# Performance work log

Hardware: AMD Instinct MI355X
Metric: run time of the kernel (lower is better)

Reference implementation:

```python
import jax, jax.numpy as jnp
import numpy as np

# dims: T tokens, HID hidden, H heads, D head_dim, K conv kernel size
T, HID, H, D, K = 4096, 2048, 16, 128, 4
HD = H * D
EPS = 1e-6


def causal_conv(x, w):
    # depthwise causal conv: x [T, C], w [C, K]; y_t = sum_i w[:, i] * x_{t-K+1+i}
    xp = jnp.pad(x, ((K - 1, 0), (0, 0)))
    y = jnp.zeros_like(x)
    for i in range(K):  # small fixed kernel loop
        y = y + w[:, i] * xp[i:i + x.shape[0]]
    return y


def l2norm(x):
    return x * jax.lax.rsqrt(jnp.sum(x * x, -1, keepdims=True) + EPS)


def setup_inputs() -> dict:
    key = jax.random.key(0)
    ks = jax.random.split(key, 16)
    s = lambda n: 1.0 / np.sqrt(n)
    return {
        "hidden_states": jax.random.normal(ks[0], (T, HID), jnp.float32),
        "Wq": jax.random.normal(ks[1], (HID, HD), jnp.float32) * s(HID),
        "Wk": jax.random.normal(ks[2], (HID, HD), jnp.float32) * s(HID),
        "Wv": jax.random.normal(ks[3], (HID, HD), jnp.float32) * s(HID),
        "wq_conv": jax.random.normal(ks[4], (HD, K), jnp.float32) * s(K),
        "wk_conv": jax.random.normal(ks[5], (HD, K), jnp.float32) * s(K),
        "wv_conv": jax.random.normal(ks[6], (HD, K), jnp.float32) * s(K),
        "A_log": jax.random.uniform(ks[7], (H,), jnp.float32, 0.0, 0.5),
        "dt_bias": jax.random.normal(ks[8], (HD,), jnp.float32) * 0.1,
        "Wfa": jax.random.normal(ks[9], (HID, D), jnp.float32) * s(HID),
        "Wfb": jax.random.normal(ks[10], (D, HD), jnp.float32) * s(D),
        "Wb": jax.random.normal(ks[11], (HID, H), jnp.float32) * s(HID),
        "Wga": jax.random.normal(ks[12], (HID, D), jnp.float32) * s(HID),
        "Wgb": jax.random.normal(ks[13], (D, HD), jnp.float32) * s(D),
        "norm_w": jnp.ones((D,), jnp.float32),
        "Wo": jax.random.normal(ks[14], (HD, HID), jnp.float32) * s(HD),
    }


def reference(hidden_states, Wq, Wk, Wv, wq_conv, wk_conv, wv_conv, A_log,
              dt_bias, Wfa, Wfb, Wb, Wga, Wgb, norm_w, Wo):
    x = hidden_states
    # projections + short causal conv + SiLU
    q = jax.nn.silu(causal_conv(x @ Wq, wq_conv)).reshape(T, H, D)
    k = jax.nn.silu(causal_conv(x @ Wk, wk_conv)).reshape(T, H, D)
    v = jax.nn.silu(causal_conv(x @ Wv, wv_conv)).reshape(T, H, D)
    # fine-grained per-channel log-decay: g = -exp(A_log) * softplus(f + dt_bias), [T,H,D]
    f = (x @ Wfa) @ Wfb + dt_bias
    g = -(jnp.exp(A_log)[None, :, None]) * jax.nn.softplus(f.reshape(T, H, D))
    beta = jax.nn.sigmoid(x @ Wb)  # [T, H]
    q = l2norm(q)
    k = l2norm(k)
    scale = D ** -0.5

    def step(S, inp):  # S: [H, Dk, Dv]
        q_t, k_t, v_t, g_t, b_t = inp
        S = S * jnp.exp(g_t)[..., None]  # diagonal per-key-channel decay
        err = v_t - jnp.einsum('hkv,hk->hv', S, k_t)  # delta-rule error
        dv = b_t[:, None] * err  # beta gate
        S = S + k_t[:, :, None] * dv[:, None, :]
        o_t = jnp.einsum('hkv,hk->hv', S, q_t) * scale
        return S, o_t

    S0 = jnp.zeros((H, D, D), jnp.float32)
    _, o = jax.lax.scan(step, S0, (q, k, v, g, beta))  # o: [T, H, D]

    # gated RMSNorm then output projection
    gate = ((x @ Wga) @ Wgb).reshape(T, H, D)
    o = o * jax.lax.rsqrt(jnp.mean(o * o, -1, keepdims=True) + EPS)
    o = o * norm_w * jax.nn.silu(gate)
    return o.reshape(T, HD) @ Wo
```

## Files before the change

kernel.cpp:

```cpp
#include <hip/hip_runtime.h>
#include <hip/hip_bf16.h>
#include <math.h>

typedef __bf16 bf16_t;
typedef __bf16 bf16x8 __attribute__((ext_vector_type(8)));
typedef float  floatx4 __attribute__((ext_vector_type(4)));
typedef float  floatx2 __attribute__((ext_vector_type(2)));
typedef unsigned uintx4 __attribute__((ext_vector_type(4)));

constexpr int T_TOK = 4096;
constexpr int HID   = 2048;
constexpr int NH    = 16;
constexpr int DH    = 128;
constexpr int CH    = 2048;
constexpr int CHUNK = 16;
constexpr int NCH   = T_TOK / CHUNK;

__global__ __launch_bounds__(256) void cast_to_bf16(const float* __restrict__ in,
                                                    bf16_t* __restrict__ out, int n) {
  int i = (blockIdx.x * 256 + threadIdx.x) * 8;
  if (i >= n) return;
  float4 a = *(const float4*)(in + i);
  float4 b = *(const float4*)(in + i + 4);
  bf16x8 o;
  o[0]=(bf16_t)a.x; o[1]=(bf16_t)a.y; o[2]=(bf16_t)a.z; o[3]=(bf16_t)a.w;
  o[4]=(bf16_t)b.x; o[5]=(bf16_t)b.y; o[6]=(bf16_t)b.z; o[7]=(bf16_t)b.w;
  *(bf16x8*)(out + i) = o;
}

__global__ __launch_bounds__(256) void transpose_cast(const float* __restrict__ in,
                                                      bf16_t* __restrict__ out, int R, int C) {
  __shared__ float tile[32][33];
  int tx = threadIdx.x & 31;
  int ty = threadIdx.x >> 5;
  int r0 = blockIdx.x * 32;
  int c0 = blockIdx.y * 32;
#pragma unroll
  for (int i = 0; i < 4; i++) {
    int r = ty + i * 8;
    float v = 0.f;
    if (r0 + r < R && c0 + tx < C) v = in[(size_t)(r0 + r) * C + (c0 + tx)];
    tile[r][tx] = v;
  }
  __syncthreads();
#pragma unroll
  for (int i = 0; i < 4; i++) {
    int cr = ty + i * 8;
    if (c0 + cr < C && r0 + tx < R)
      out[(size_t)(c0 + cr) * R + (r0 + tx)] = (bf16_t)tile[tx][cr];
  }
}

template<bool OUT_BF16>
__global__ __launch_bounds__(256) void gemm_bf16(
    const bf16_t* __restrict__ A, int lda,
    const bf16_t* __restrict__ Bt, int ldb,
    void* __restrict__ Cv, int ldc, int M, int N, int K) {
  __shared__ bf16_t sA[128][40];
  __shared__ bf16_t sB[128][40];
  const int tid  = threadIdx.x;
  const int bm0  = blockIdx.x * 128;
  const int bn0  = blockIdx.y * 128;
  const int wave = tid >> 6;
  const int lane = tid & 63;
  const int wm   = (wave & 1) * 64;
  const int wn   = (wave >> 1) * 64;
  const int fm   = lane & 15;
  const int kq   = lane >> 4;

  floatx4 acc[4][4];
#pragma unroll
  for (int mi = 0; mi < 4; mi++)
#pragma unroll
    for (int ni = 0; ni < 4; ni++)
      acc[mi][ni] = (floatx4){0.f, 0.f, 0.f, 0.f};

  const int sr = tid >> 2;
  const int sk = (tid & 3) * 8;
  const bool bval0 = (bn0 + sr) < N;
  const bool bval1 = (bn0 + sr + 64) < N;
  const bf16_t* Ag0 = A + (size_t)(bm0 + sr) * lda + sk;
  const bf16_t* Ag1 = Ag0 + (size_t)64 * lda;
  const bf16_t* Bg0 = Bt + (size_t)(bn0 + sr) * ldb + sk;
  const bf16_t* Bg1 = Bg0 + (size_t)64 * ldb;

  for (int k0 = 0; k0 < K; k0 += 32) {
    float4 a0 = *(const float4*)(Ag0 + k0);
    float4 a1 = *(const float4*)(Ag1 + k0);
    float4 b0 = bval0 ? *(const float4*)(Bg0 + k0) : make_float4(0.f, 0.f, 0.f, 0.f);
    float4 b1 = bval1 ? *(const float4*)(Bg1 + k0) : make_float4(0.f, 0.f, 0.f, 0.f);
    __syncthreads();
    *(float4*)(&sA[sr][sk])      = a0;
    *(float4*)(&sA[sr + 64][sk]) = a1;
    *(float4*)(&sB[sr][sk])      = b0;
    *(float4*)(&sB[sr + 64][sk]) = b1;
    __syncthreads();
    bf16x8 afr[4], bfr[4];
#pragma unroll
    for (int i = 0; i < 4; i++) {
      afr[i] = *(const bf16x8*)(&sA[wm + i * 16 + fm][kq * 8]);
      bfr[i] = *(const bf16x8*)(&sB[wn + i * 16 + fm][kq * 8]);
    }
#pragma unroll
    for (int mi = 0; mi < 4; mi++)
#pragma unroll
      for (int ni = 0; ni < 4; ni++)
        acc[mi][ni] = __builtin_amdgcn_mfma_f32_16x16x32_bf16(afr[mi], bfr[ni], acc[mi][ni], 0, 0, 0);
  }

  const int rr = (lane >> 4) * 4;
#pragma unroll
  for (int mi = 0; mi < 4; mi++) {
#pragma unroll
    for (int r = 0; r < 4; r++) {
      const int row = bm0 + wm + mi * 16 + rr + r;
#pragma unroll
      for (int ni = 0; ni < 4; ni++) {
        const int col = bn0 + wn + ni * 16 + fm;
        if (col < N) {
          if constexpr (OUT_BF16)
            ((bf16_t*)Cv)[(size_t)row * ldc + col] = (bf16_t)acc[mi][ni][r];
          else
            ((float*)Cv)[(size_t)row * ldc + col] = acc[mi][ni][r];
        }
      }
    }
  }
}

__device__ __forceinline__ void gload_lds16(const bf16_t* g, bf16_t* l) {
  __builtin_amdgcn_global_load_lds(
      (const __attribute__((address_space(1))) void*)g,
      (__attribute__((address_space(3))) void*)l, 16, 0, 0);
}

template<bool OUT_BF16>
__global__ __launch_bounds__(256) void gemm_bf16_lds(
    const bf16_t* __restrict__ A, int lda,
    const bf16_t* __restrict__ Bt, int ldb,
    void* __restrict__ Cv, int ldc, int M, int N, int K) {
  __shared__ bf16_t sA[128][32];
  __shared__ bf16_t sB[128][32];
  const int tid  = threadIdx.x;
  const int bm0  = blockIdx.x * 128;
  const int bn0  = blockIdx.y * 128;
  const int wave = tid >> 6;
  const int lane = tid & 63;
  const int wm   = (wave & 1) * 64;
  const int wn   = (wave >> 1) * 64;
  const int fm   = lane & 15;
  const int kq   = lane >> 4;

  floatx4 acc[4][4];
#pragma unroll
  for (int mi = 0; mi < 4; mi++)
#pragma unroll
    for (int ni = 0; ni < 4; ni++)
      acc[mi][ni] = (floatx4){0.f, 0.f, 0.f, 0.f};

  const int sr = tid >> 2;
  const int sk = (tid & 3) * 8;
  const bf16_t* Ag0 = A + (size_t)(bm0 + sr) * lda + sk;
  const bf16_t* Ag1 = Ag0 + (size_t)64 * lda;
  const bf16_t* Bg0 = Bt + (size_t)(bn0 + sr) * ldb + sk;
  const bf16_t* Bg1 = Bg0 + (size_t)64 * ldb;
  bf16_t* ldsA0 = &sA[16 * wave][0];
  bf16_t* ldsA1 = &sA[64 + 16 * wave][0];
  bf16_t* ldsB0 = &sB[16 * wave][0];
  bf16_t* ldsB1 = &sB[64 + 16 * wave][0];

  for (int k0 = 0; k0 < K; k0 += 32) {
    __syncthreads();
    gload_lds16(Ag0 + k0, ldsA0);
    gload_lds16(Ag1 + k0, ldsA1);
    gload_lds16(Bg0 + k0, ldsB0);
    gload_lds16(Bg1 + k0, ldsB1);
    __syncthreads();
    bf16x8 afr[4], bfr[4];
#pragma unroll
    for (int i = 0; i < 4; i++) {
      afr[i] = *(const bf16x8*)(&sA[wm + i * 16 + fm][kq * 8]);
      bfr[i] = *(const bf16x8*)(&sB[wn + i * 16 + fm][kq * 8]);
    }
#pragma unroll
    for (int mi = 0; mi < 4; mi++)
#pragma unroll
      for (int ni = 0; ni < 4; ni++)
        acc[mi][ni] = __builtin_amdgcn_mfma_f32_16x16x32_bf16(afr[mi], bfr[ni], acc[mi][ni], 0, 0, 0);
  }

  const int rr = (lane >> 4) * 4;
#pragma unroll
  for (int mi = 0; mi < 4; mi++) {
#pragma unroll
    for (int r = 0; r < 4; r++) {
      const int row = bm0 + wm + mi * 16 + rr + r;
#pragma unroll
      for (int ni = 0; ni < 4; ni++) {
        const int col = bn0 + wn + ni * 16 + fm;
        if constexpr (OUT_BF16)
          ((bf16_t*)Cv)[(size_t)row * ldc + col] = (bf16_t)acc[mi][ni][r];
        else
          ((float*)Cv)[(size_t)row * ldc + col] = acc[mi][ni][r];
      }
    }
  }
}

template<bool L2NORM>
__global__ __launch_bounds__(256) void conv_silu(
    const bf16_t* __restrict__ raw, const float* __restrict__ wconv,
    bf16_t* __restrict__ out) {
  const int t   = blockIdx.x;
  const int tid = threadIdx.x;
  const int c0  = tid * 8;

  float w[8][4];
#pragma unroll
  for (int j = 0; j < 8; j++) {
    float4 t0 = *(const float4*)(wconv + (size_t)(c0 + j) * 4);
    w[j][0] = t0.x; w[j][1] = t0.y; w[j][2] = t0.z; w[j][3] = t0.w;
  }
  float a[8] = {};
#pragma unroll
  for (int i = 0; i < 4; i++) {
    int tr = t - 3 + i;
    if (tr < 0) continue;
    bf16x8 xr = *(const bf16x8*)(raw + (size_t)tr * CH + c0);
#pragma unroll
    for (int j = 0; j < 8; j++) a[j] += w[j][i] * (float)xr[j];
  }
  float s = 0.f;
#pragma unroll
  for (int j = 0; j < 8; j++) {
    a[j] = a[j] / (1.f + expf(-a[j]));
    s += a[j] * a[j];
  }
  float rs = 1.f;
  if constexpr (L2NORM) {
#pragma unroll
    for (int m = 1; m < 16; m <<= 1) s += __shfl_xor(s, m);
    rs = rsqrtf(s + 1e-6f);
  }
  bf16x8 r;
#pragma unroll
  for (int j = 0; j < 8; j++) r[j] = (bf16_t)(a[j] * rs);
  *(bf16x8*)(out + (size_t)t * CH + c0) = r;
}

__global__ __launch_bounds__(256) void gamma_beta(
    float* __restrict__ f_gam, const float* __restrict__ dt_bias,
    const float* __restrict__ A_log, float* __restrict__ beta_io) {
  const int t   = blockIdx.x;
  const int tid = threadIdx.x;
  const int c0  = tid * 8;
  const int h   = c0 >> 7;
  const float a_h = expf(A_log[h]);
  const size_t o0 = (size_t)t * CH + c0;
  float fv[8], db[8];
  { float4 f0 = *(const float4*)(f_gam + o0);   float4 f1 = *(const float4*)(f_gam + o0 + 4);
    fv[0]=f0.x; fv[1]=f0.y; fv[2]=f0.z; fv[3]=f0.w; fv[4]=f1.x; fv[5]=f1.y; fv[6]=f1.z; fv[7]=f1.w;
    float4 d0 = *(const float4*)(dt_bias + c0); float4 d1 = *(const float4*)(dt_bias + c0 + 4);
    db[0]=d0.x; db[1]=d0.y; db[2]=d0.z; db[3]=d0.w; db[4]=d1.x; db[5]=d1.y; db[6]=d1.z; db[7]=d1.w; }
  float og[8];
#pragma unroll
  for (int j = 0; j < 8; j++) {
    float f = fv[j] + db[j];
    float sp = (f > 20.f) ? f : log1pf(expf(f));
    og[j] = -a_h * sp;
  }
  *(float4*)(f_gam + o0)     = make_float4(og[0], og[1], og[2], og[3]);
  *(float4*)(f_gam + o0 + 4) = make_float4(og[4], og[5], og[6], og[7]);
  if (tid < NH) {
    float b = beta_io[(size_t)t * NH + tid];
    beta_io[(size_t)t * NH + tid] = 1.f / (1.f + expf(-b));
  }
}

template<int IMM>
__device__ __forceinline__ float swzf(float x) {
  return __builtin_bit_cast(float, __builtin_amdgcn_ds_swizzle(__builtin_bit_cast(int, x), IMM));
}
template<int CTRL>
__device__ __forceinline__ float dppadd(float x) {
  int v = __builtin_amdgcn_update_dpp(0, __builtin_bit_cast(int, x), CTRL, 0xF, 0xF, true);
  return x + __builtin_bit_cast(float, v);
}
__device__ __forceinline__ float cumsum16(float x) {
  x = dppadd<0x111>(x);
  x = dppadd<0x112>(x);
  x = dppadd<0x114>(x);
  x = dppadd<0x118>(x);
  return x;
}
__device__ __forceinline__ float bperm(int lane, float x) {
  return __builtin_bit_cast(float, __builtin_amdgcn_ds_bpermute(lane << 2, __builtin_bit_cast(int, x)));
}
__device__ __forceinline__ floatx2 bfpair(unsigned u) {
  floatx2 r;
  r[0] = __builtin_bit_cast(float, u << 16);
  r[1] = __builtin_bit_cast(float, u & 0xFFFF0000u);
  return r;
}

__global__ __launch_bounds__(64) void wy_prep(
    bf16_t* __restrict__ qn, bf16_t* __restrict__ kn,
    const float* __restrict__ gg, const float* __restrict__ beta,
    bf16_t* __restrict__ ktilT, float* __restrict__ Tm,
    bf16_t* __restrict__ MBf, float* __restrict__ ecT, float* __restrict__ e2T) {
  const int hc = blockIdx.x;
  const int h  = hc >> 8;
  const int c  = hc & 255;
  const int l  = threadIdx.x;
  const int tl = l & 15;
  const int gr = l >> 4;

  __shared__ bf16_t KldsT[128][24];
  __shared__ float  Wlds[16][17];
  __shared__ float  Mlds[16][17];
  __shared__ float  eclds[128], e2lds[128];
  __shared__ float  blds[16];

  const int kb0 = h * DH + gr * 8;
  const size_t rowoff = (size_t)(c * CHUNK + tl) * CH;

  if (gr == 0) blds[tl] = beta[(size_t)(c * CHUNK + tl) * NH + h];

  floatx4 wt = (floatx4){0.f, 0.f, 0.f, 0.f};
  floatx4 m  = (floatx4){0.f, 0.f, 0.f, 0.f};
  bf16x8 khs[4], qhs[4];
#pragma unroll
  for (int kb = 0; kb < 4; kb++) {
    const int ke = kb0 + kb * 32;
    float4 ga = *(const float4*)(gg + rowoff + ke);
    float4 gb = *(const float4*)(gg + rowoff + ke + 4);
    float cm[8] = {ga.x, ga.y, ga.z, ga.w, gb.x, gb.y, gb.z, gb.w};
    float lamh[8], lamt[8], ec[8], e2[8];
#pragma unroll
    for (int j = 0; j < 8; j++) {
      float cs   = cumsum16(cm[j]);
      float cmid = swzf<(7 << 5) | 0x10>(cs);
      lamh[j] = __expf(cs - cmid);
      lamt[j] = __expf(cmid - cs);
      ec[j]   = __expf(cmid);
      e2[j]   = swzf<(15 << 5) | 0x10>(lamh[j]);
    }
    if (tl == 0) {
#pragma unroll
      for (int j = 0; j < 8; j++) {
        eclds[kb * 32 + gr * 8 + j] = ec[j];
        e2lds[kb * 32 + gr * 8 + j] = e2[j];
      }
    }
    uint4 kr = *(const uint4*)(kn + rowoff + ke);
    uint4 qr = *(const uint4*)(qn + rowoff + ke);
    float kf[8], qf[8];
    { floatx2 a0 = bfpair(kr.x), a1 = bfpair(kr.y), a2 = bfpair(kr.z), a3 = bfpair(kr.w);
      kf[0]=a0[0];kf[1]=a0[1];kf[2]=a1[0];kf[3]=a1[1];kf[4]=a2[0];kf[5]=a2[1];kf[6]=a3[0];kf[7]=a3[1];
      floatx2 b0 = bfpair(qr.x), b1 = bfpair(qr.y), b2 = bfpair(qr.z), b3 = bfpair(qr.w);
      qf[0]=b0[0];qf[1]=b0[1];qf[2]=b1[0];qf[3]=b1[1];qf[4]=b2[0];qf[5]=b2[1];qf[6]=b3[0];qf[7]=b3[1]; }
    bf16x8 khat, ktil, qhat;
#pragma unroll
    for (int j = 0; j < 8; j++) {
      khat[j] = (bf16_t)(kf[j] * lamh[j]);
      ktil[j] = (bf16_t)(kf[j] * lamt[j]);
      qhat[j] = (bf16_t)(qf[j] * lamh[j]);
      khs[kb][j] = (bf16_t)(kf[j] * lamh[j] * ec[j]);
      qhs[kb][j] = (bf16_t)(qf[j] * lamh[j] * ec[j]);
    }
    wt = __builtin_amdgcn_mfma_f32_16x16x32_bf16(ktil, khat, wt, 0, 0, 0);
    m  = __builtin_amdgcn_mfma_f32_16x16x32_bf16(qhat, ktil, m,  0, 0, 0);
#pragma unroll
    for (int j = 0; j < 8; j++) KldsT[kb * 32 + gr * 8 + j][tl] = ktil[j];
  }
#pragma unroll
  for (int kb = 0; kb < 4; kb++) {
    *(uint4*)(kn + rowoff + kb0 + kb * 32) = __builtin_bit_cast(uint4, khs[kb]);
    *(uint4*)(qn + rowoff + kb0 + kb * 32) = __builtin_bit_cast(uint4, qhs[kb]);
  }
#pragma unroll
  for (int ri = 0; ri < 4; ri++) {
    Wlds[tl][4 * gr + ri] = wt[ri];
    Mlds[4 * gr + ri][tl] = (4 * gr + ri >= tl) ? m[ri] : 0.f;
  }
  {
    const int j = tl;
    float x[16];
#pragma unroll
    for (int t = 0; t < 16; t++) {
      float a = 0.f;
#pragma unroll
      for (int s = 0; s < 16; s++)
        if (s < t) a = fmaf(Wlds[t][s], x[s], a);
      x[t] = (t == j) ? 1.f : ((t > j) ? -blds[t] * a : 0.f);
    }
    if (gr == 0) {
      const float bj = blds[j];
#pragma unroll
      for (int t = 0; t < 16; t++)
        Tm[((size_t)hc * 16 + t) * 16 + j] = x[t] * bj;
    }
  }
  {
    uint4 mbo = {0, 0, 0, 0};
    if (gr < 2) {
      bf16x8 mm;
#pragma unroll
      for (int jj = 0; jj < 8; jj++) mm[jj] = (bf16_t)Mlds[tl][gr * 8 + jj];
      mbo = __builtin_bit_cast(uint4, mm);
    }
    ((uint4*)MBf)[(size_t)hc * 64 + l] = mbo;
  }
  for (int i = l; i < 128; i += 64) {
    uint4 a0 = *(const uint4*)&KldsT[i][0];
    uint4 a1 = *(const uint4*)&KldsT[i][8];
    bf16_t* dst = ktilT + ((size_t)hc * 128 + i) * 16;
    *(uint4*)dst = a0;
    *(uint4*)(dst + 8) = a1;
  }
  for (int i = l; i < 128; i += 64) {
    ecT[(size_t)hc * 128 + (i & 15) * 8 + (i >> 4)] = eclds[i];
    e2T[(size_t)hc * 128 + (i & 15) * 8 + (i >> 4)] = e2lds[i];
  }
}

__global__ __launch_bounds__(128, 1) void scan_wy3(
    const bf16_t* __restrict__ khsG, const bf16_t* __restrict__ qhsG,
    const bf16_t* __restrict__ vn, const bf16_t* __restrict__ ktilT,
    const float* __restrict__ Tm, const bf16_t* __restrict__ MBf,
    const float* __restrict__ ecT, const float* __restrict__ e2T,
    float* __restrict__ o) {
  const int h   = blockIdx.x >> 3;
  const int vt  = blockIdx.x & 7;
  const int tid = threadIdx.x;
  const int wid = tid >> 6;
  const int l   = tid & 63;
  const int tl  = l & 15;
  const int gr  = l >> 4;

  __shared__ uint4   sKQ[2][8][64];
  __shared__ floatx4 sT[2][4][64];
  __shared__ uint4   sMB[2][64];
  __shared__ uint4   sKT[2][8][64];
  __shared__ floatx4 sEC[2][4][64];
  __shared__ uint2   sV[2][64];
  __shared__ float   SldsT[16][132];
  __shared__ float   DVlds[16][17];

  const int kb0 = h * DH + gr * 8;
  const int vb0 = h * DH + vt * 16 + gr * 4;
  const size_t hcBase = (size_t)h * NCH;
  constexpr float scale = 0.08838834764831845f;

  auto produce = [&](int c, int b) {
    const size_t rowoff = (size_t)(c * CHUNK + tl) * CH;
    const size_t hc = hcBase + c;
    uint4 kq[8];
#pragma unroll
    for (int kb = 0; kb < 4; kb++) {
      kq[kb]     = *(const uint4*)(khsG + rowoff + kb0 + kb * 32);
      kq[4 + kb] = *(const uint4*)(qhsG + rowoff + kb0 + kb * 32);
    }
    const float* Trp = Tm + (hc * 16 + tl) * 16;
    floatx4 Tv[4];
#pragma unroll
    for (int j = 0; j < 4; j++) Tv[j] = *(const floatx4*)(Trp + 4 * j);
    uint4 mbv = ((const uint4*)MBf)[hc * 64 + l];
    const int g2 = gr & 1;
    uint4 ktv[8];
#pragma unroll
    for (int kt = 0; kt < 8; kt++)
      ktv[kt] = *(const uint4*)(ktilT + (hc * 128 + kt * 16 + tl) * 16 + g2 * 8);
    floatx4 ecv[4];
    ecv[0] = *(const floatx4*)(ecT + hc * 128 + tl * 8);
    ecv[1] = *(const floatx4*)(ecT + hc * 128 + tl * 8 + 4);
    ecv[2] = *(const floatx4*)(e2T + hc * 128 + tl * 8);
    ecv[3] = *(const floatx4*)(e2T + hc * 128 + tl * 8 + 4);
    uint2 vv = *(const uint2*)(vn + rowoff + vb0);
#pragma unroll
    for (int i = 0; i < 8; i++) sKQ[b][i][l] = kq[i];
#pragma unroll
    for (int j = 0; j < 4; j++) sT[b][j][l] = Tv[j];
    sMB[b][l] = mbv;
#pragma unroll
    for (int i = 0; i < 8; i++) sKT[b][i][l] = ktv[i];
#pragma unroll
    for (int j = 0; j < 4; j++) sEC[b][j][l] = ecv[j];
    sV[b][l] = vv;
  };

  float S[8][4];
#pragma unroll
  for (int kt = 0; kt < 8; kt++)
#pragma unroll
    for (int ri = 0; ri < 4; ri++) S[kt][ri] = 0.f;

  if (wid == 1) {
    produce(0, 0);
  } else {
    for (int i = l; i < 16 * 132; i += 64) (&SldsT[0][0])[i] = 0.f;
  }
  __syncthreads();

  int cur = 0;
  for (int c = 0; c < NCH; ++c) {
    if (wid == 1) {
      produce(c + 1 < NCH ? c + 1 : NCH - 1, cur ^ 1);
    } else {
      const size_t rowoff = (size_t)(c * CHUNK + tl) * CH;
      floatx4 p  = (floatx4){0.f, 0.f, 0.f, 0.f};
      floatx4 o1 = (floatx4){0.f, 0.f, 0.f, 0.f};
#pragma unroll
      for (int kb = 0; kb < 4; kb++) {
        float4 sa = *(const float4*)(&SldsT[tl][kb * 32 + gr * 8]);
        float4 sb = *(const float4*)(&SldsT[tl][kb * 32 + gr * 8 + 4]);
        bf16x8 s0a;
        s0a[0]=(bf16_t)sa.x; s0a[1]=(bf16_t)sa.y; s0a[2]=(bf16_t)sa.z; s0a[3]=(bf16_t)sa.w;
        s0a[4]=(bf16_t)sb.x; s0a[5]=(bf16_t)sb.y; s0a[6]=(bf16_t)sb.z; s0a[7]=(bf16_t)sb.w;
        p  = __builtin_amdgcn_mfma_f32_16x16x32_bf16(s0a, __builtin_bit_cast(bf16x8, sKQ[cur][kb][l]), p,  0, 0, 0);
        o1 = __builtin_amdgcn_mfma_f32_16x16x32_bf16(s0a, __builtin_bit_cast(bf16x8, sKQ[cur][4 + kb][l]), o1, 0, 0, 0);
      }
      float acc[4];
      { uint2 vr = sV[cur][l];
        floatx2 v01 = bfpair(vr.x), v23 = bfpair(vr.y);
        acc[0] = v01[0] - p[0]; acc[1] = v01[1] - p[1];
        acc[2] = v23[0] - p[2]; acc[3] = v23[1] - p[3]; }
      *(float4*)(&DVlds[tl][4 * gr]) = make_float4(acc[0], acc[1], acc[2], acc[3]);
      floatx4 T0 = sT[cur][0][l], T1 = sT[cur][1][l], T2 = sT[cur][2][l], T3 = sT[cur][3][l];
      float dv[4] = {0.f, 0.f, 0.f, 0.f};
#pragma unroll
      for (int s = 0; s < 16; s++) {
        const float ts = (s < 4) ? T0[s] : (s < 8) ? T1[s - 4] : (s < 12) ? T2[s - 8] : T3[s - 12];
        float4 vp = *(const float4*)(&DVlds[s][4 * gr]);
        dv[0] = fmaf(ts, vp.x, dv[0]);
        dv[1] = fmaf(ts, vp.y, dv[1]);
        dv[2] = fmaf(ts, vp.z, dv[2]);
        dv[3] = fmaf(ts, vp.w, dv[3]);
      }
#pragma unroll
      for (int ri = 0; ri < 4; ri++) DVlds[tl][4 * gr + ri] = dv[ri];
      bf16x8 dva = {};
      if (gr < 2) {
#pragma unroll
        for (int jj = 0; jj < 8; jj++) dva[jj] = (bf16_t)DVlds[gr * 8 + jj][tl];
      }
      floatx4 o2 = __builtin_amdgcn_mfma_f32_16x16x32_bf16(
          dva, __builtin_bit_cast(bf16x8, sMB[cur][l]), (floatx4){0.f, 0.f, 0.f, 0.f}, 0, 0, 0);
      { float4 ov = make_float4((o1[0] + o2[0]) * scale, (o1[1] + o2[1]) * scale,
                                (o1[2] + o2[2]) * scale, (o1[3] + o2[3]) * scale);
        *(float4*)(o + rowoff + vb0) = ov; }
      floatx4 ec0 = sEC[cur][0][l], ec1 = sEC[cur][1][l];
      floatx4 e20 = sEC[cur][2][l], e21 = sEC[cur][3][l];
#pragma unroll
      for (int kt = 0; kt < 8; kt++) {
        const float ecK = (kt < 4) ? ec0[kt] : ec1[kt - 4];
        const float e2K = (kt < 4) ? e20[kt] : e21[kt - 4];
        floatx4 sa;
#pragma unroll
        for (int ri = 0; ri < 4; ri++) sa[ri] = ecK * S[kt][ri];
        sa = __builtin_amdgcn_mfma_f32_16x16x32_bf16(
            dva, __builtin_bit_cast(bf16x8, sKT[cur][kt][l]), sa, 0, 0, 0);
#pragma unroll
        for (int ri = 0; ri < 4; ri++) S[kt][ri] = e2K * sa[ri];
      }
#pragma unroll
      for (int kt = 0; kt < 8; kt++)
#pragma unroll
        for (int ri = 0; ri < 4; ri++)
          SldsT[4 * gr + ri][kt * 16 + tl] = S[kt][ri];
    }
    __syncthreads();
    cur ^= 1;
  }
}

__global__ __launch_bounds__(256) void postprocess(
    const float* __restrict__ o, const bf16_t* __restrict__ gate,
    const float* __restrict__ norm_w, bf16_t* __restrict__ og) {
  const int t = blockIdx.x, tid = threadIdx.x;
  const int c0 = tid * 8, d0 = c0 & 127;
  const size_t o0 = (size_t)t * CH + c0;
  float ov[8], gv[8], nw[8];
  { float4 a = *(const float4*)(o + o0);    float4 b = *(const float4*)(o + o0 + 4);
    ov[0]=a.x; ov[1]=a.y; ov[2]=a.z; ov[3]=a.w; ov[4]=b.x; ov[5]=b.y; ov[6]=b.z; ov[7]=b.w;
    bf16x8 g8 = *(const bf16x8*)(gate + o0);
    for (int j = 0; j < 8; j++) gv[j] = (float)g8[j];
    float4 e = *(const float4*)(norm_w + d0); float4 f = *(const float4*)(norm_w + d0 + 4);
    nw[0]=e.x; nw[1]=e.y; nw[2]=e.z; nw[3]=e.w; nw[4]=f.x; nw[5]=f.y; nw[6]=f.z; nw[7]=f.w; }
  float ss = 0.f;
#pragma unroll
  for (int j = 0; j < 8; j++) ss += ov[j] * ov[j];
#pragma unroll
  for (int m = 1; m < 16; m <<= 1) ss += __shfl_xor(ss, m);
  const float rs = rsqrtf(ss * (1.f / 128.f) + 1e-6f);
  bf16x8 r;
#pragma unroll
  for (int j = 0; j < 8; j++) {
    float g = gv[j];
    float val = ov[j] * rs * nw[j] * (g / (1.f + expf(-g)));
    r[j] = (bf16_t)val;
  }
  *(bf16x8*)(og + o0) = r;
}

static inline void launch_gemm(const bf16_t* A, int lda, const bf16_t* Bt, int ldb,
                               void* C, int ldc, int M, int N, int K, bool obf16,
                               hipStream_t s) {
  dim3 grid(M / 128, (N + 127) / 128);
  if ((N & 127) == 0) {
    if (obf16) gemm_bf16_lds<true><<<grid, 256, 0, s>>>(A, lda, Bt, ldb, C, ldc, M, N, K);
    else       gemm_bf16_lds<false><<<grid, 256, 0, s>>>(A, lda, Bt, ldb, C, ldc, M, N, K);
  } else {
    if (obf16) gemm_bf16<true><<<grid, 256, 0, s>>>(A, lda, Bt, ldb, C, ldc, M, N, K);
    else       gemm_bf16<false><<<grid, 256, 0, s>>>(A, lda, Bt, ldb, C, ldc, M, N, K);
  }
}

extern "C" void kernel_launch(void* const* d_in, const int* in_sizes, int n_in,
                              void* d_out, int out_size, void* d_ws, size_t ws_size,
                              hipStream_t stream) {
  const float* x       = (const float*)d_in[0];
  const float* Wq      = (const float*)d_in[1];
  const float* Wk      = (const float*)d_in[2];
  const float* Wv      = (const float*)d_in[3];
  const float* wqc     = (const float*)d_in[4];
  const float* wkc     = (const float*)d_in[5];
  const float* wvc     = (const float*)d_in[6];
  const float* A_log   = (const float*)d_in[7];
  const float* dt_bias = (const float*)d_in[8];
  const float* Wfa     = (const float*)d_in[9];
  const float* Wfb     = (const float*)d_in[10];
  const float* Wb      = (const float*)d_in[11];
  const float* Wga     = (const float*)d_in[12];
  const float* Wgb     = (const float*)d_in[13];
  const float* norm_w  = (const float*)d_in[14];
  const float* Wo      = (const float*)d_in[15];

  char* w = (char*)d_ws;
  size_t off = 0;
  auto give = [&](size_t bytes) -> void* {
    size_t cur = off;
    off = (off + bytes + 255) & ~(size_t)255;
    return (void*)(w + cur);
  };
  bf16_t* Wbig = (bf16_t*)give((size_t)CH * HID * 2);
  bf16_t* WfaT = (bf16_t*)give((size_t)128 * HID * 2);
  bf16_t* WgaT = (bf16_t*)give((size_t)128 * HID * 2);
  bf16_t* WfbT = (bf16_t*)give((size_t)CH * 128 * 2);
  bf16_t* WgbT = (bf16_t*)give((size_t)CH * 128 * 2);
  bf16_t* WbT  = (bf16_t*)give((size_t)NH * HID * 2);
  bf16_t* Ax   = (bf16_t*)give((size_t)T_TOK * HID * 2);
  bf16_t* raw0 = (bf16_t*)give((size_t)T_TOK * CH * 2);
  bf16_t* qnb  = (bf16_t*)give((size_t)T_TOK * CH * 2);
  bf16_t* knb  = (bf16_t*)give((size_t)T_TOK * CH * 2);
  bf16_t* vnb  = (bf16_t*)give((size_t)T_TOK * CH * 2);
  bf16_t* f1b  = (bf16_t*)give((size_t)T_TOK * 128 * 2);
  bf16_t* g1b  = (bf16_t*)give((size_t)T_TOK * 128 * 2);
  float*  fbuf = (float*)give((size_t)T_TOK * CH * 4);
  bf16_t* gateb= (bf16_t*)give((size_t)T_TOK * CH * 2);
  float*  betab= (float*)give((size_t)T_TOK * NH * 4);
  bf16_t* ktilT= (bf16_t*)give((size_t)NH * NCH * 128 * 16 * 2);
  float*  Tmat = (float*)give((size_t)NH * NCH * 256 * 4);
  bf16_t* MBf  = (bf16_t*)give((size_t)NH * NCH * 64 * 8 * 2);
  float*  ecTb = (float*)give((size_t)NH * NCH * 128 * 4);
  float*  e2Tb = (float*)give((size_t)NH * NCH * 128 * 4);
  float*  obuf = (float*)Ax;
  bf16_t* ogb  = qnb;

  auto tr = [&](const float* in, bf16_t* out, int R, int C) {
    transpose_cast<<<dim3((R + 31) / 32, (C + 31) / 32), 256, 0, stream>>>(in, out, R, C);
  };

  cast_to_bf16<<<dim3((T_TOK * HID) / 2048), 256, 0, stream>>>(x, Ax, T_TOK * HID);
  tr(Wfa, WfaT, HID, 128); tr(Wga, WgaT, HID, 128);
  tr(Wfb, WfbT, 128, CH);  tr(Wgb, WgbT, 128, CH);
  tr(Wb, WbT, HID, NH);

  tr(Wq, Wbig, HID, CH);
  launch_gemm(Ax, HID, Wbig, HID, raw0, CH, T_TOK, CH, HID, true, stream);
  conv_silu<true><<<dim3(T_TOK), 256, 0, stream>>>(raw0, wqc, qnb);
  tr(Wk, Wbig, HID, CH);
  launch_gemm(Ax, HID, Wbig, HID, raw0, CH, T_TOK, CH, HID, true, stream);
  conv_silu<true><<<dim3(T_TOK), 256, 0, stream>>>(raw0, wkc, knb);
  tr(Wv, Wbig, HID, CH);
  launch_gemm(Ax, HID, Wbig, HID, raw0, CH, T_TOK, CH, HID, true, stream);
  conv_silu<false><<<dim3(T_TOK), 256, 0, stream>>>(raw0, wvc, vnb);

  launch_gemm(Ax, HID, WfaT, HID, f1b, 128, T_TOK, 128, HID, true, stream);
  launch_gemm(Ax, HID, WgaT, HID, g1b, 128, T_TOK, 128, HID, true, stream);
  launch_gemm(Ax, HID, WbT, HID, betab, NH, T_TOK, NH, HID, false, stream);
  launch_gemm(f1b, 128, WfbT, 128, fbuf, CH, T_TOK, CH, 128, false, stream);
  launch_gemm(g1b, 128, WgbT, 128, gateb, CH, T_TOK, CH, 128, true, stream);
  gamma_beta<<<dim3(T_TOK), 256, 0, stream>>>(fbuf, dt_bias, A_log, betab);

  wy_prep<<<dim3(NH * NCH), 64, 0, stream>>>(qnb, knb, fbuf, betab,
                                             ktilT, Tmat, MBf, ecTb, e2Tb);
  scan_wy3<<<dim3(128), 128, 0, stream>>>(knb, qnb, vnb, ktilT, Tmat, MBf,
                                          ecTb, e2Tb, obuf);

  postprocess<<<dim3(T_TOK), 256, 0, stream>>>(obuf, gateb, norm_w, ogb);

  tr(Wo, Wbig, CH, HID);
  launch_gemm(ogb, CH, Wbig, CH, (float*)d_out, HID, T_TOK, HID, CH, false, stream);
}
```

Baseline: 1.025 ms.

## Double-buffer GEMM LDS tiles, defer scan output stores, fuse low-rank projections

The LDS-staged GEMM now keeps two tile buffers and prefetches the next K-slice while computing on the current one, which cuts two barriers per iteration down to one. In the scan kernel, compute waves write outputs to shared memory and the producer wave stores them to global one chunk later, taking global stores off the serial critical path. The Wfa and Wga down-projections are merged into a single N=256 GEMM with one concatenated weight buffer. This costs more shared memory per block, which may lower occupancy, and relies on the async LDS loads being correctly ordered by the single barrier.

```diff
diff --git a/kernel.cpp b/kernel.cpp
--- a/kernel.cpp
+++ b/kernel.cpp
@@ -139,8 +139,8 @@
     const bf16_t* __restrict__ A, int lda,
     const bf16_t* __restrict__ Bt, int ldb,
     void* __restrict__ Cv, int ldc, int M, int N, int K) {
-  __shared__ bf16_t sA[128][32];
-  __shared__ bf16_t sB[128][32];
+  __shared__ bf16_t sA[2][128][32];
+  __shared__ bf16_t sB[2][128][32];
   const int tid  = threadIdx.x;
   const int bm0  = blockIdx.x * 128;
   const int bn0  = blockIdx.y * 128;
@@ -164,29 +164,32 @@
   const bf16_t* Ag1 = Ag0 + (size_t)64 * lda;
   const bf16_t* Bg0 = Bt + (size_t)(bn0 + sr) * ldb + sk;
   const bf16_t* Bg1 = Bg0 + (size_t)64 * ldb;
-  bf16_t* ldsA0 = &sA[16 * wave][0];
-  bf16_t* ldsA1 = &sA[64 + 16 * wave][0];
-  bf16_t* ldsB0 = &sB[16 * wave][0];
-  bf16_t* ldsB1 = &sB[64 + 16 * wave][0];
-
+
+  auto stage = [&](int b, int k0) {
+    gload_lds16(Ag0 + k0, &sA[b][16 * wave][0]);
+    gload_lds16(Ag1 + k0, &sA[b][64 + 16 * wave][0]);
+    gload_lds16(Bg0 + k0, &sB[b][16 * wave][0]);
+    gload_lds16(Bg1 + k0, &sB[b][64 + 16 * wave][0]);
+  };
+
+  stage(0, 0);
+  __syncthreads();
+  int cur = 0;
   for (int k0 = 0; k0 < K; k0 += 32) {
-    __syncthreads();
-    gload_lds16(Ag0 + k0, ldsA0);
-    gload_lds16(Ag1 + k0, ldsA1);
-    gload_lds16(Bg0 + k0, ldsB0);
-    gload_lds16(Bg1 + k0, ldsB1);
-    __syncthreads();
+    if (k0 + 32 < K) stage(cur ^ 1, k0 + 32);
     bf16x8 afr[4], bfr[4];
 #pragma unroll
     for (int i = 0; i < 4; i++) {
-      afr[i] = *(const bf16x8*)(&sA[wm + i * 16 + fm][kq * 8]);
-      bfr[i] = *(const bf16x8*)(&sB[wn + i * 16 + fm][kq * 8]);
+      afr[i] = *(const bf16x8*)(&sA[cur][wm + i * 16 + fm][kq * 8]);
+      bfr[i] = *(const bf16x8*)(&sB[cur][wn + i * 16 + fm][kq * 8]);
     }
 #pragma unroll
     for (int mi = 0; mi < 4; mi++)
 #pragma unroll
       for (int ni = 0; ni < 4; ni++)
         acc[mi][ni] = __builtin_amdgcn_mfma_f32_16x16x32_bf16(afr[mi], bfr[ni], acc[mi][ni], 0, 0, 0);
+    __syncthreads();
+    cur ^= 1;
   }
 
   const int rr = (lane >> 4) * 4;
@@ -293,9 +296,6 @@
   x = dppadd<0x118>(x);
   return x;
 }
-__device__ __forceinline__ float bperm(int lane, float x) {
-  return __builtin_bit_cast(float, __builtin_amdgcn_ds_bpermute(lane << 2, __builtin_bit_cast(int, x)));
-}
 __device__ __forceinline__ floatx2 bfpair(unsigned u) {
   floatx2 r;
   r[0] = __builtin_bit_cast(float, u << 16);
@@ -444,6 +444,7 @@
   __shared__ uint4   sKT[2][8][64];
   __shared__ floatx4 sEC[2][4][64];
   __shared__ uint2   sV[2][64];
+  __shared__ float4  sO[2][64];
   __shared__ float   SldsT[16][132];
   __shared__ float   DVlds[16][17];
 
@@ -505,9 +506,13 @@
   int cur = 0;
   for (int c = 0; c < NCH; ++c) {
     if (wid == 1) {
+      if (c >= 1) {
+        float4 ov = sO[cur ^ 1][l];
+        const size_t rowp = (size_t)((c - 1) * CHUNK + tl) * CH;
+        *(float4*)(o + rowp + vb0) = ov;
+      }
       produce(c + 1 < NCH ? c + 1 : NCH - 1, cur ^ 1);
     } else {
-      const size_t rowoff = (size_t)(c * CHUNK + tl) * CH;
       floatx4 p  = (floatx4){0.f, 0.f, 0.f, 0.f};
       floatx4 o1 = (floatx4){0.f, 0.f, 0.f, 0.f};
 #pragma unroll
@@ -546,9 +551,8 @@
       }
       floatx4 o2 = __builtin_amdgcn_mfma_f32_16x16x32_bf16(
           dva, __builtin_bit_cast(bf16x8, sMB[cur][l]), (floatx4){0.f, 0.f, 0.f, 0.f}, 0, 0, 0);
-      { float4 ov = make_float4((o1[0] + o2[0]) * scale, (o1[1] + o2[1]) * scale,
-                                (o1[2] + o2[2]) * scale, (o1[3] + o2[3]) * scale);
-        *(float4*)(o + rowoff + vb0) = ov; }
+      sO[cur][l] = make_float4((o1[0] + o2[0]) * scale, (o1[1] + o2[1]) * scale,
+                               (o1[2] + o2[2]) * scale, (o1[3] + o2[3]) * scale);
       floatx4 ec0 = sEC[cur][0][l], ec1 = sEC[cur][1][l];
       floatx4 e20 = sEC[cur][2][l], e21 = sEC[cur][3][l];
 #pragma unroll
@@ -571,6 +575,11 @@
     }
     __syncthreads();
     cur ^= 1;
+  }
+  if (wid == 1) {
+    float4 ov = sO[(NCH - 1) & 1][l];
+    const size_t rowp = (size_t)((NCH - 1) * CHUNK + tl) * CH;
+    *(float4*)(o + rowp + vb0) = ov;
   }
 }
 
@@ -644,8 +653,7 @@
     return (void*)(w + cur);
   };
   bf16_t* Wbig = (bf16_t*)give((size_t)CH * HID * 2);
-  bf16_t* WfaT = (bf16_t*)give((size_t)128 * HID * 2);
-  bf16_t* WgaT = (bf16_t*)give((size_t)128 * HID * 2);
+  bf16_t* WfgT = (bf16_t*)give((size_t)256 * HID * 2);
   bf16_t* WfbT = (bf16_t*)give((size_t)CH * 128 * 2);
   bf16_t* WgbT = (bf16_t*)give((size_t)CH * 128 * 2);
   bf16_t* WbT  = (bf16_t*)give((size_t)NH * HID * 2);
@@ -654,8 +662,7 @@
   bf16_t* qnb  = (bf16_t*)give((size_t)T_TOK * CH * 2);
   bf16_t* knb  = (bf16_t*)give((size_t)T_TOK * CH * 2);
   bf16_t* vnb  = (bf16_t*)give((size_t)T_TOK * CH * 2);
-  bf16_t* f1b  = (bf16_t*)give((size_t)T_TOK * 128 * 2);
-  bf16_t* g1b  = (bf16_t*)give((size_t)T_TOK * 128 * 2);
+  bf16_t* f1g1 = (bf16_t*)give((size_t)T_TOK * 256 * 2);
   float*  fbuf = (float*)give((size_t)T_TOK * CH * 4);
   bf16_t* gateb= (bf16_t*)give((size_t)T_TOK * CH * 2);
   float*  betab= (float*)give((size_t)T_TOK * NH * 4);
@@ -672,7 +679,8 @@
   };
 
   cast_to_bf16<<<dim3((T_TOK * HID) / 2048), 256, 0, stream>>>(x, Ax, T_TOK * HID);
-  tr(Wfa, WfaT, HID, 128); tr(Wga, WgaT, HID, 128);
+  tr(Wfa, WfgT, HID, 128);
+  tr(Wga, WfgT + (size_t)128 * HID, HID, 128);
   tr(Wfb, WfbT, 128, CH);  tr(Wgb, WgbT, 128, CH);
   tr(Wb, WbT, HID, NH);
 
@@ -686,11 +694,10 @@
   launch_gemm(Ax, HID, Wbig, HID, raw0, CH, T_TOK, CH, HID, true, stream);
   conv_silu<false><<<dim3(T_TOK), 256, 0, stream>>>(raw0, wvc, vnb);
 
-  launch_gemm(Ax, HID, WfaT, HID, f1b, 128, T_TOK, 128, HID, true, stream);
-  launch_gemm(Ax, HID, WgaT, HID, g1b, 128, T_TOK, 128, HID, true, stream);
+  launch_gemm(Ax, HID, WfgT, HID, f1g1, 256, T_TOK, 256, HID, true, stream);
   launch_gemm(Ax, HID, WbT, HID, betab, NH, T_TOK, NH, HID, false, stream);
-  launch_gemm(f1b, 128, WfbT, 128, fbuf, CH, T_TOK, CH, 128, false, stream);
-  launch_gemm(g1b, 128, WgbT, 128, gateb, CH, T_TOK, CH, 128, true, stream);
+  launch_gemm(f1g1, 256, WfbT, 128, fbuf, CH, T_TOK, CH, 128, false, stream);
+  launch_gemm(f1g1 + 128, 256, WgbT, 128, gateb, CH, T_TOK, CH, 128, true, stream);
   gamma_beta<<<dim3(T_TOK), 256, 0, stream>>>(fbuf, dt_bias, A_log, betab);
 
   wy_prep<<<dim3(NH * NCH), 64, 0, stream>>>(qnb, knb, fbuf, betab,
```

New measurement: 958.2 us. -6.5%, faster.
